# Kernel tuning notes

Measured on AMD Instinct MI355X. Metric: run time of the kernel, lower is better.

## Reference

```python
import jax, jax.numpy as jnp
import numpy as np

N = 100000          # nodes
E = 1600000         # edges (avg degree 16)
F_IN = 128          # num_node_features
H = 128             # hidden_channels
C = 8               # num_classes
EPS = 1e-5          # batchnorm eps
SLOPE = 0.01        # leaky_relu negative slope


def setup_inputs() -> dict:
    key = jax.random.key(0)
    ks = jax.random.split(key, 12)
    s = 0.05
    inp = {
        "node_feat": jax.random.normal(ks[0], (N, F_IN), jnp.float32),
        "src": jax.random.randint(ks[1], (E,), 0, N, dtype=jnp.int32),
        "dst": jax.random.randint(ks[2], (E,), 0, N, dtype=jnp.int32),
        # conv1 / conv2 (GraphConv weights + bias)
        "W1": jax.random.normal(ks[3], (F_IN, H), jnp.float32) * s,
        "b1": jnp.zeros((H,), jnp.float32),
        "W2": jax.random.normal(ks[4], (H, H), jnp.float32) * s,
        "b2": jnp.zeros((H,), jnp.float32),
        # batchnorm affine params
        "gamma1": jnp.ones((H,), jnp.float32),
        "beta1": jnp.zeros((H,), jnp.float32),
        "gamma2": jnp.ones((H,), jnp.float32),
        "beta2": jnp.zeros((H,), jnp.float32),
        # convnode1 / convnode2
        "Wn1": jax.random.normal(ks[5], (H, H), jnp.float32) * s,
        "bn1": jnp.zeros((H,), jnp.float32),
        "Wn2": jax.random.normal(ks[6], (H, H), jnp.float32) * s,
        "bn2": jnp.zeros((H,), jnp.float32),
        # node classifier
        "Wc": jax.random.normal(ks[7], (H, C), jnp.float32) * s,
        "bc": jnp.zeros((C,), jnp.float32),
    }
    return inp


def _deg_inv_sqrt(idx):
    # clamp(deg, min=1) ** -0.5, as in DGL GraphConv norm='both'
    deg = jax.ops.segment_sum(jnp.ones((E,), jnp.float32), idx, num_segments=N)
    return jnp.clip(deg, 1.0, None) ** -0.5


def _gconv(x, src, dst, W, b, out_norm, in_norm):
    # DGL GraphConv, norm='both': gather src-normalized feats, scatter-add to dst,
    # normalize by in-degree, then dense transform.
    msg = (x * out_norm[:, None])[src]                    # [E, d] gather
    agg = jax.ops.segment_sum(msg, dst, num_segments=N)   # [N, d] scatter-add
    return (agg * in_norm[:, None]) @ W + b


def _bn(x, gamma, beta):
    # training-mode BatchNorm1d: batch mean / biased var
    mean = jnp.mean(x, axis=0)
    var = jnp.var(x, axis=0)
    return (x - mean) * jax.lax.rsqrt(var + EPS) * gamma + beta


def _lrelu(x):
    return jnp.where(x >= 0, x, SLOPE * x)


def reference(node_feat, src, dst, W1, b1, W2, b2, gamma1, beta1, gamma2, beta2,
              Wn1, bn1, Wn2, bn2, Wc, bc):
    out_norm = _deg_inv_sqrt(src)   # src out-degree norm
    in_norm = _deg_inv_sqrt(dst)    # dst in-degree norm

    h = _gconv(node_feat, src, dst, W1, b1, out_norm, in_norm)
    h = _lrelu(_bn(h, gamma1, beta1))
    h = _gconv(h, src, dst, W2, b2, out_norm, in_norm)
    h = _lrelu(_bn(h, gamma2, beta2))

    hn = _lrelu(_gconv(h, src, dst, Wn1, bn1, out_norm, in_norm))
    hn = _lrelu(_gconv(hn, src, dst, Wn2, bn2, out_norm, in_norm))

    return hn @ Wc + bc   # [N, C]
```

## Files before the change

kernel.cpp:

```cpp
#include <hip/hip_runtime.h>
#include <math.h>

#define HN 128
#define NC 8
#define EPSV 1e-5f
#define SLOPEV 0.01f

typedef __attribute__((ext_vector_type(4))) float f32x4;
typedef __attribute__((ext_vector_type(8))) short bf16x8;

__device__ __forceinline__ uint bf16rne(float f) {
    uint u = __float_as_uint(f);
    return (u + 0x7fffu + ((u >> 16) & 1u)) >> 16;
}

__global__ __launch_bounds__(256) void rank_kernel(
        const int* __restrict__ src, const int* __restrict__ dst,
        int* __restrict__ degO, int* __restrict__ cntI,
        int* __restrict__ rnk, int E) {
    int base = blockIdx.x * 1024 + threadIdx.x;
    int s[4], d[4], r[4];
    #pragma unroll
    for (int k = 0; k < 4; k++) {
        int e = base + k * 256;
        if (e < E) { s[k] = src[e]; d[k] = dst[e]; }
    }
    #pragma unroll
    for (int k = 0; k < 4; k++) {
        int e = base + k * 256;
        if (e < E) atomicAdd(&degO[s[k]], 1);
    }
    #pragma unroll
    for (int k = 0; k < 4; k++) {
        int e = base + k * 256;
        if (e < E) r[k] = atomicAdd(&cntI[d[k]], 1);
    }
    #pragma unroll
    for (int k = 0; k < 4; k++) {
        int e = base + k * 256;
        if (e < E) rnk[e] = r[k];
    }
}

__global__ __launch_bounds__(256) void scan_partial(const int* __restrict__ degI,
                                                    int* __restrict__ blockSums, int n) {
    __shared__ int sS[256];
    int tid = threadIdx.x;
    int base = blockIdx.x * 1024 + tid * 4;
    int s = 0;
    #pragma unroll
    for (int j = 0; j < 4; j++) {
        int idx = base + j;
        s += (idx < n) ? degI[idx] : 0;
    }
    sS[tid] = s;
    __syncthreads();
    for (int off = 128; off; off >>= 1) {
        if (tid < off) sS[tid] += sS[tid + off];
        __syncthreads();
    }
    if (tid == 0) blockSums[blockIdx.x] = sS[0];
}

__global__ __launch_bounds__(1024) void scan_blocksums(int* __restrict__ blockSums, int nb) {
    __shared__ int sS[1024];
    int tid = threadIdx.x;
    int v = (tid < nb) ? blockSums[tid] : 0;
    sS[tid] = v;
    __syncthreads();
    for (int off = 1; off < 1024; off <<= 1) {
        int t = (tid >= off) ? sS[tid - off] : 0;
        __syncthreads();
        sS[tid] += t;
        __syncthreads();
    }
    if (tid < nb) blockSums[tid] = sS[tid] - v;
}

__global__ __launch_bounds__(256) void scan_final(const int* __restrict__ degI,
                                                  const int* __restrict__ degO,
                                                  const int* __restrict__ blockSums,
                                                  int* __restrict__ row_ptr,
                                                  float* __restrict__ onorm,
                                                  float* __restrict__ inorm, int n, int E) {
    __shared__ int sS[256];
    int tid = threadIdx.x;
    int base = blockIdx.x * 1024 + tid * 4;
    int v[4];
    int tot = 0;
    #pragma unroll
    for (int j = 0; j < 4; j++) {
        int idx = base + j;
        int vv = (idx < n) ? degI[idx] : 0;
        v[j] = tot;
        tot += vv;
    }
    sS[tid] = tot;
    __syncthreads();
    for (int off = 1; off < 256; off <<= 1) {
        int t = (tid >= off) ? sS[tid - off] : 0;
        __syncthreads();
        sS[tid] += t;
        __syncthreads();
    }
    int tb = blockSums[blockIdx.x] + sS[tid] - tot;
    #pragma unroll
    for (int j = 0; j < 4; j++) {
        int idx = base + j;
        if (idx < n) {
            row_ptr[idx] = tb + v[j];
            float a = (float)degO[idx]; if (a < 1.f) a = 1.f;
            float b = (float)degI[idx]; if (b < 1.f) b = 1.f;
            onorm[idx] = rsqrtf(a);
            inorm[idx] = rsqrtf(b);
        }
    }
    if (blockIdx.x == 0 && tid == 0) row_ptr[n] = E;
}

__global__ __launch_bounds__(256) void scatter_kernel(
        const int* __restrict__ src, const int* __restrict__ dst,
        const int* __restrict__ rnk, const int* __restrict__ row_ptr,
        int* __restrict__ srcs, int E) {
    int base = blockIdx.x * 1024 + threadIdx.x;
    int s[4], d[4], r[4], rp[4];
    #pragma unroll
    for (int k = 0; k < 4; k++) {
        int e = base + k * 256;
        if (e < E) { d[k] = dst[e]; r[k] = rnk[e]; s[k] = src[e]; }
    }
    #pragma unroll
    for (int k = 0; k < 4; k++) {
        int e = base + k * 256;
        if (e < E) rp[k] = row_ptr[d[k]];
    }
    #pragma unroll
    for (int k = 0; k < 4; k++) {
        int e = base + k * 256;
        if (e < E) srcs[rp[k] + r[k]] = s[k];
    }
}

__global__ __launch_bounds__(256) void wprep_kernel(
        const float* __restrict__ W1, const float* __restrict__ W2,
        const float* __restrict__ W3, const float* __restrict__ W4,
        ushort* __restrict__ WTh, ushort* __restrict__ WTl) {
    int i = blockIdx.x * blockDim.x + threadIdx.x;
    int l = i >> 14, r = i & 16383;
    int k = r >> 7, nn = r & 127;
    const float* W = (l == 0) ? W1 : (l == 1) ? W2 : (l == 2) ? W3 : W4;
    float w = W[k * HN + nn];
    uint hi = bf16rne(w);
    float fhi = __uint_as_float(hi << 16);
    uint lo = bf16rne(w - fhi);
    WTh[(size_t)l * 16384 + nn * HN + k] = (ushort)hi;
    WTl[(size_t)l * 16384 + nn * HN + k] = (ushort)lo;
}

__global__ __launch_bounds__(256) void pack_kernel(
        const float* __restrict__ in, const float* __restrict__ onorm,
        ushort* __restrict__ out, int total4) {
    int i = blockIdx.x * blockDim.x + threadIdx.x;
    if (i >= total4) return;
    float w = onorm[i >> 5];
    float4 v = ((const float4*)in)[i];
    ushort4 o = make_ushort4((ushort)bf16rne(v.x * w), (ushort)bf16rne(v.y * w),
                             (ushort)bf16rne(v.z * w), (ushort)bf16rne(v.w * w));
    *(ushort4*)(out + (size_t)i * 4) = o;
}

__global__ __launch_bounds__(256) void bnpack_kernel(
        const float* __restrict__ in, ushort* __restrict__ out,
        const float* __restrict__ scale, const float* __restrict__ shift,
        const float* __restrict__ onorm, int total4) {
    int i = blockIdx.x * blockDim.x + threadIdx.x;
    if (i >= total4) return;
    int cp = (i & 31) << 2;
    float w = onorm[i >> 5];
    float4 v = ((const float4*)in)[i];
    float4 s = *(const float4*)(scale + cp);
    float4 t = *(const float4*)(shift + cp);
    float h0 = fmaf(v.x, s.x, t.x); h0 = (h0 >= 0.f) ? h0 : SLOPEV * h0;
    float h1 = fmaf(v.y, s.y, t.y); h1 = (h1 >= 0.f) ? h1 : SLOPEV * h1;
    float h2 = fmaf(v.z, s.z, t.z); h2 = (h2 >= 0.f) ? h2 : SLOPEV * h2;
    float h3 = fmaf(v.w, s.w, t.w); h3 = (h3 >= 0.f) ? h3 : SLOPEV * h3;
    ushort4 o = make_ushort4((ushort)bf16rne(h0 * w), (ushort)bf16rne(h1 * w),
                             (ushort)bf16rne(h2 * w), (ushort)bf16rne(h3 * w));
    *(ushort4*)(out + (size_t)i * 4) = o;
}

__global__ __launch_bounds__(256) void agg_kernel(
        const uint* __restrict__ xb, uint* __restrict__ out,
        const int* __restrict__ srcs, const int* __restrict__ row_ptr,
        const float* __restrict__ inorm, int n) {
    int node = blockIdx.x * 4 + (threadIdx.x >> 6);
    if (node >= n) return;
    int lane = threadIdx.x & 63;
    int rp0 = row_ptr[node], rp1 = row_ptr[node + 1];
    float accx = 0.f, accy = 0.f;
    int j = rp0;
    for (; j + 3 < rp1; j += 4) {
        int s0 = srcs[j], s1 = srcs[j + 1], s2 = srcs[j + 2], s3 = srcs[j + 3];
        uint u0 = xb[(size_t)s0 * 64 + lane];
        uint u1 = xb[(size_t)s1 * 64 + lane];
        uint u2 = xb[(size_t)s2 * 64 + lane];
        uint u3 = xb[(size_t)s3 * 64 + lane];
        accx += __uint_as_float(u0 << 16) + __uint_as_float(u1 << 16)
              + __uint_as_float(u2 << 16) + __uint_as_float(u3 << 16);
        accy += __uint_as_float(u0 & 0xffff0000u) + __uint_as_float(u1 & 0xffff0000u)
              + __uint_as_float(u2 & 0xffff0000u) + __uint_as_float(u3 & 0xffff0000u);
    }
    for (; j < rp1; j++) {
        uint u0 = xb[(size_t)srcs[j] * 64 + lane];
        accx += __uint_as_float(u0 << 16);
        accy += __uint_as_float(u0 & 0xffff0000u);
    }
    float wi = inorm[node];
    uint o = bf16rne(accx * wi) | (bf16rne(accy * wi) << 16);
    out[(size_t)node * 64 + lane] = o;
}

template<int DO_STATS, int DO_LRELU, int DO_PACK, int DO_CLS>
__global__ __launch_bounds__(512) void gemm_mfma(
        const ushort* __restrict__ A, const uint4* __restrict__ WTh4,
        const uint4* __restrict__ WTl4, const float* __restrict__ bias,
        void* __restrict__ outv, float* __restrict__ colsum, float* __restrict__ colsq,
        const float* __restrict__ onorm,
        const float* __restrict__ Wc, const float* __restrict__ bc, int n) {
    __shared__ uint4 sW[4096];
    int tid = threadIdx.x;
    #pragma unroll
    for (int it = 0; it < 4; it++) {
        int j = it * 512 + tid;
        int nrow = j >> 4, c = j & 15;
        int sidx = nrow * 16 + (c ^ (nrow & 15));
        sW[sidx] = WTh4[j];
        sW[2048 + sidx] = WTl4[j];
    }
    __syncthreads();

    int wave = tid >> 6, lane = tid & 63;
    int l15 = lane & 15, quad = lane >> 4;
    int rbase = blockIdx.x * 128 + wave * 16;
    int arow = rbase + l15; if (arow > n - 1) arow = n - 1;

    bf16x8 af[4];
    #pragma unroll
    for (int kc = 0; kc < 4; kc++)
        af[kc] = *(const bf16x8*)(A + (size_t)arow * HN + kc * 32 + quad * 8);

    f32x4 acc[8];
    #pragma unroll
    for (int t = 0; t < 8; t++) acc[t] = (f32x4){0.f, 0.f, 0.f, 0.f};

    #pragma unroll
    for (int t = 0; t < 8; t++) {
        int nn = t * 16 + l15;
        int base = nn * 16, sw = nn & 15;
        #pragma unroll
        for (int kc = 0; kc < 4; kc++) {
            int c = kc * 4 + quad;
            bf16x8 bh = *(const bf16x8*)&sW[base + (c ^ sw)];
            acc[t] = __builtin_amdgcn_mfma_f32_16x16x32_bf16(af[kc], bh, acc[t], 0, 0, 0);
        }
        #pragma unroll
        for (int kc = 0; kc < 4; kc++) {
            int c = kc * 4 + quad;
            bf16x8 bl = *(const bf16x8*)&sW[2048 + base + (c ^ sw)];
            acc[t] = __builtin_amdgcn_mfma_f32_16x16x32_bf16(af[kc], bl, acc[t], 0, 0, 0);
        }
    }

    if (DO_CLS) {
        float bvt[8];
        #pragma unroll
        for (int t = 0; t < 8; t++) bvt[t] = bias[t * 16 + l15];
        #pragma unroll
        for (int c = 0; c < NC; c++) {
            float cl[4] = {0.f, 0.f, 0.f, 0.f};
            #pragma unroll
            for (int t = 0; t < 8; t++) {
                float wcv = Wc[(t * 16 + l15) * NC + c];
                #pragma unroll
                for (int i = 0; i < 4; i++) {
                    float v = acc[t][i] + bvt[t];
                    v = (v >= 0.f) ? v : SLOPEV * v;
                    cl[i] = fmaf(v, wcv, cl[i]);
                }
            }
            #pragma unroll
            for (int i = 0; i < 4; i++) {
                cl[i] += __shfl_xor(cl[i], 1);
                cl[i] += __shfl_xor(cl[i], 2);
                cl[i] += __shfl_xor(cl[i], 4);
                cl[i] += __shfl_xor(cl[i], 8);
            }
            if (l15 == 0) {
                float bcv = bc[c];
                #pragma unroll
                for (int i = 0; i < 4; i++) {
                    int row = rbase + quad * 4 + i;
                    if (row < n) ((float*)outv)[(size_t)row * NC + c] = cl[i] + bcv;
                }
            }
        }
        return;
    }

    float sarr[8], qarr[8];
    #pragma unroll
    for (int t = 0; t < 8; t++) {
        int col = t * 16 + l15;
        float bv = bias[col];
        float s = 0.f, q = 0.f;
        #pragma unroll
        for (int i = 0; i < 4; i++) {
            int row = rbase + quad * 4 + i;
            float v = acc[t][i] + bv;
            if (DO_LRELU) v = (v >= 0.f) ? v : SLOPEV * v;
            if (row < n) {
                if (DO_PACK) {
                    ((ushort*)outv)[(size_t)row * HN + col] = (ushort)bf16rne(v * onorm[row]);
                } else {
                    ((float*)outv)[(size_t)row * HN + col] = v;
                }
                if (DO_STATS) { s += v; q += v * v; }
            }
        }
        if (DO_STATS) {
            s += __shfl_xor(s, 16); q += __shfl_xor(q, 16);
            s += __shfl_xor(s, 32); q += __shfl_xor(q, 32);
        }
        sarr[t] = s; qarr[t] = q;
    }

    if (DO_STATS) {
        __syncthreads();
        float* sSum = (float*)sW;
        float* sSq  = (float*)sW + 1024;
        if (quad == 0) {
            #pragma unroll
            for (int t = 0; t < 8; t++) {
                sSum[wave * 128 + t * 16 + l15] = sarr[t];
                sSq [wave * 128 + t * 16 + l15] = qarr[t];
            }
        }
        __syncthreads();
        if (tid < 128) {
            float s = 0.f, q = 0.f;
            #pragma unroll
            for (int w = 0; w < 8; w++) { s += sSum[w * 128 + tid]; q += sSq[w * 128 + tid]; }
            atomicAdd(&colsum[tid], s);
            atomicAdd(&colsq[tid], q);
        }
    }
}

__global__ void bn_finalize(const float* __restrict__ colsum, const float* __restrict__ colsq,
                            const float* __restrict__ gamma, const float* __restrict__ beta,
                            float* __restrict__ scale, float* __restrict__ shift, int n) {
    int c = threadIdx.x;
    if (c < HN) {
        float inv = 1.f / (float)n;
        float mean = colsum[c] * inv;
        float var = colsq[c] * inv - mean * mean;
        if (var < 0.f) var = 0.f;
        float s = gamma[c] * rsqrtf(var + EPSV);
        scale[c] = s;
        shift[c] = beta[c] - mean * s;
    }
}

extern "C" void kernel_launch(void* const* d_in, const int* in_sizes, int n_in,
                              void* d_out, int out_size, void* d_ws, size_t ws_size,
                              hipStream_t stream) {
    const float* node_feat = (const float*)d_in[0];
    const int*   src    = (const int*)d_in[1];
    const int*   dst    = (const int*)d_in[2];
    const float* W1     = (const float*)d_in[3];
    const float* b1     = (const float*)d_in[4];
    const float* W2     = (const float*)d_in[5];
    const float* b2     = (const float*)d_in[6];
    const float* gamma1 = (const float*)d_in[7];
    const float* beta1  = (const float*)d_in[8];
    const float* gamma2 = (const float*)d_in[9];
    const float* beta2  = (const float*)d_in[10];
    const float* Wn1    = (const float*)d_in[11];
    const float* bn1    = (const float*)d_in[12];
    const float* Wn2    = (const float*)d_in[13];
    const float* bn2    = (const float*)d_in[14];
    const float* Wc     = (const float*)d_in[15];
    const float* bc     = (const float*)d_in[16];
    float* out = (float*)d_out;

    const int N = in_sizes[0] / HN;
    const int E = in_sizes[1];

    char* p = (char*)d_ws;
    float* bufA  = (float*)p; p += (size_t)N * HN * 4;
    float* bufB  = (float*)p; p += (size_t)N * HN * 4;
    float* onorm = (float*)p; p += (size_t)N * 4;
    float* inorm = (float*)p; p += (size_t)N * 4;
    float* scale = (float*)p; p += HN * 4;
    float* shift = (float*)p; p += HN * 4;
    char* zbase = p;
    float* cs1 = (float*)p; p += HN * 4;
    float* cq1 = (float*)p; p += HN * 4;
    float* cs2 = (float*)p; p += HN * 4;
    float* cq2 = (float*)p; p += HN * 4;
    int* degO = (int*)p; p += (size_t)N * 4;
    int* cntI = (int*)p; p += (size_t)N * 4;
    size_t zbytes = (size_t)(p - zbase);
    int* row_ptr = (int*)p; p += (size_t)(N + 4) * 4;
    int* blockSums = (int*)p; p += 1024 * 4;
    int* rnk     = (int*)p; p += (size_t)E * 4;
    int* srcs    = (int*)p; p += (size_t)E * 4;
    ushort* WTh  = (ushort*)p; p += 4 * 16384 * 2;
    ushort* WTl  = (ushort*)p; p += 4 * 16384 * 2;
    if ((size_t)(p - (char*)d_ws) > ws_size) return;

    hipMemsetAsync(zbase, 0, zbytes, stream);

    int gE4 = (E + 1023) / 1024;
    int nb = (N + 1023) / 1024;
    rank_kernel<<<gE4, 256, 0, stream>>>(src, dst, degO, cntI, rnk, E);
    scan_partial<<<nb, 256, 0, stream>>>(cntI, blockSums, N);
    scan_blocksums<<<1, 1024, 0, stream>>>(blockSums, nb);
    scan_final<<<nb, 256, 0, stream>>>(cntI, degO, blockSums, row_ptr, onorm, inorm, N, E);
    scatter_kernel<<<gE4, 256, 0, stream>>>(src, dst, rnk, row_ptr, srcs, E);
    wprep_kernel<<<256, 256, 0, stream>>>(W1, W2, Wn1, Wn2, WTh, WTl);

    int gAgg = (N + 3) / 4;
    int gGemm = (N + 127) / 128;
    int gApply = (N * 32 + 255) / 256;

    ushort* HbA = (ushort*)bufA;
    ushort* Abf = (ushort*)bufA + (size_t)N * HN;
    ushort* HbB = (ushort*)bufB;

    pack_kernel<<<gApply, 256, 0, stream>>>(node_feat, onorm, HbA, N * 32);
    agg_kernel<<<gAgg, 256, 0, stream>>>((const uint*)HbA, (uint*)Abf, srcs, row_ptr, inorm, N);
    gemm_mfma<1, 0, 0, 0><<<gGemm, 512, 0, stream>>>(Abf, (const uint4*)WTh, (const uint4*)WTl,
                                                     b1, bufB, cs1, cq1, nullptr, nullptr, nullptr, N);
    bn_finalize<<<1, 128, 0, stream>>>(cs1, cq1, gamma1, beta1, scale, shift, N);
    bnpack_kernel<<<gApply, 256, 0, stream>>>(bufB, HbA, scale, shift, onorm, N * 32);

    agg_kernel<<<gAgg, 256, 0, stream>>>((const uint*)HbA, (uint*)Abf, srcs, row_ptr, inorm, N);
    gemm_mfma<1, 0, 0, 0><<<gGemm, 512, 0, stream>>>(Abf, (const uint4*)(WTh + 16384),
                                                     (const uint4*)(WTl + 16384),
                                                     b2, bufB, cs2, cq2, nullptr, nullptr, nullptr, N);
    bn_finalize<<<1, 128, 0, stream>>>(cs2, cq2, gamma2, beta2, scale, shift, N);
    bnpack_kernel<<<gApply, 256, 0, stream>>>(bufB, HbA, scale, shift, onorm, N * 32);

    agg_kernel<<<gAgg, 256, 0, stream>>>((const uint*)HbA, (uint*)Abf, srcs, row_ptr, inorm, N);
    gemm_mfma<0, 1, 1, 0><<<gGemm, 512, 0, stream>>>(Abf, (const uint4*)(WTh + 2 * 16384),
                                                     (const uint4*)(WTl + 2 * 16384),
                                                     bn1, HbB, nullptr, nullptr, onorm, nullptr, nullptr, N);

    agg_kernel<<<gAgg, 256, 0, stream>>>((const uint*)HbB, (uint*)Abf, srcs, row_ptr, inorm, N);
    gemm_mfma<0, 0, 0, 1><<<gGemm, 512, 0, stream>>>(Abf, (const uint4*)(WTh + 3 * 16384),
                                                     (const uint4*)(WTl + 3 * 16384),
                                                     bn2, out, nullptr, nullptr, nullptr, Wc, bc, N);
}
```

Before: 799.8 us.

## Split packed features into two column halves and use per-XCC degree counters

Packed bf16 feature buffers are stored as two planar 64-column halves, so each aggregation pass gathers 128-byte rows from one half at a time. Work is split across twice as many blocks, each wave handling two edges per step with 32 lanes each and combining via a cross-lane shuffle. The intent is a smaller gather working set per pass, for better L2 reuse and more memory parallelism. Out-degree counting is also privatized per XCC using workgroup-scope atomics, with the eight copies summed in scan_final, to cut cross-die atomic traffic. The risks are more index arithmetic, half-wasted lanes on low-degree nodes, and atomic-scope correctness relying on the XCC ID register.

```diff
diff --git a/kernel.cpp b/kernel.cpp
--- a/kernel.cpp
+++ b/kernel.cpp
@@ -14,10 +14,17 @@
     return (u + 0x7fffu + ((u >> 16) & 1u)) >> 16;
 }
 
+__device__ __forceinline__ int xcc_id() {
+    int x;
+    asm volatile("s_getreg_b32 %0, hwreg(HW_REG_XCC_ID)" : "=s"(x));
+    return x & 7;
+}
+
 __global__ __launch_bounds__(256) void rank_kernel(
         const int* __restrict__ src, const int* __restrict__ dst,
-        int* __restrict__ degO, int* __restrict__ cntI,
-        int* __restrict__ rnk, int E) {
+        int* __restrict__ degO8, int* __restrict__ cntI,
+        int* __restrict__ rnk, int E, int n) {
+    int* myDeg = degO8 + (size_t)xcc_id() * n;
     int base = blockIdx.x * 1024 + threadIdx.x;
     int s[4], d[4], r[4];
     #pragma unroll
@@ -28,7 +35,9 @@
     #pragma unroll
     for (int k = 0; k < 4; k++) {
         int e = base + k * 256;
-        if (e < E) atomicAdd(&degO[s[k]], 1);
+        if (e < E)
+            __hip_atomic_fetch_add(&myDeg[s[k]], 1, __ATOMIC_RELAXED,
+                                   __HIP_MEMORY_SCOPE_WORKGROUP);
     }
     #pragma unroll
     for (int k = 0; k < 4; k++) {
@@ -78,7 +87,7 @@
 }
 
 __global__ __launch_bounds__(256) void scan_final(const int* __restrict__ degI,
-                                                  const int* __restrict__ degO,
+                                                  const int* __restrict__ degO8,
                                                   const int* __restrict__ blockSums,
                                                   int* __restrict__ row_ptr,
                                                   float* __restrict__ onorm,
@@ -109,7 +118,10 @@
         int idx = base + j;
         if (idx < n) {
             row_ptr[idx] = tb + v[j];
-            float a = (float)degO[idx]; if (a < 1.f) a = 1.f;
+            int dsum = 0;
+            #pragma unroll
+            for (int s8 = 0; s8 < 8; s8++) dsum += degO8[(size_t)s8 * n + idx];
+            float a = (float)dsum; if (a < 1.f) a = 1.f;
             float b = (float)degI[idx]; if (b < 1.f) b = 1.f;
             onorm[idx] = rsqrtf(a);
             inorm[idx] = rsqrtf(b);
@@ -159,24 +171,27 @@
 
 __global__ __launch_bounds__(256) void pack_kernel(
         const float* __restrict__ in, const float* __restrict__ onorm,
-        ushort* __restrict__ out, int total4) {
+        ushort* __restrict__ out, int nrows) {
     int i = blockIdx.x * blockDim.x + threadIdx.x;
-    if (i >= total4) return;
-    float w = onorm[i >> 5];
+    if (i >= nrows * 32) return;
+    int row = i >> 5, q4 = i & 31;
+    float w = onorm[row];
     float4 v = ((const float4*)in)[i];
     ushort4 o = make_ushort4((ushort)bf16rne(v.x * w), (ushort)bf16rne(v.y * w),
                              (ushort)bf16rne(v.z * w), (ushort)bf16rne(v.w * w));
-    *(ushort4*)(out + (size_t)i * 4) = o;
+    int h = q4 >> 4, lc = (q4 * 2) & 31;
+    *(ushort4*)(out + (((size_t)h * nrows + row) * 32 + lc) * 2) = o;
 }
 
 __global__ __launch_bounds__(256) void bnpack_kernel(
         const float* __restrict__ in, ushort* __restrict__ out,
         const float* __restrict__ scale, const float* __restrict__ shift,
-        const float* __restrict__ onorm, int total4) {
+        const float* __restrict__ onorm, int nrows) {
     int i = blockIdx.x * blockDim.x + threadIdx.x;
-    if (i >= total4) return;
-    int cp = (i & 31) << 2;
-    float w = onorm[i >> 5];
+    if (i >= nrows * 32) return;
+    int row = i >> 5, q4 = i & 31;
+    int cp = q4 << 2;
+    float w = onorm[row];
     float4 v = ((const float4*)in)[i];
     float4 s = *(const float4*)(scale + cp);
     float4 t = *(const float4*)(shift + cp);
@@ -186,38 +201,46 @@
     float h3 = fmaf(v.w, s.w, t.w); h3 = (h3 >= 0.f) ? h3 : SLOPEV * h3;
     ushort4 o = make_ushort4((ushort)bf16rne(h0 * w), (ushort)bf16rne(h1 * w),
                              (ushort)bf16rne(h2 * w), (ushort)bf16rne(h3 * w));
-    *(ushort4*)(out + (size_t)i * 4) = o;
+    int h = q4 >> 4, lc = (q4 * 2) & 31;
+    *(ushort4*)(out + (((size_t)h * nrows + row) * 32 + lc) * 2) = o;
 }
 
 __global__ __launch_bounds__(256) void agg_kernel(
-        const uint* __restrict__ xb, uint* __restrict__ out,
+        const uint* __restrict__ xb, uint* __restrict__ outb,
         const int* __restrict__ srcs, const int* __restrict__ row_ptr,
-        const float* __restrict__ inorm, int n) {
-    int node = blockIdx.x * 4 + (threadIdx.x >> 6);
+        const float* __restrict__ inorm, int n, int nodeBlocks) {
+    int h = blockIdx.x / nodeBlocks;
+    int nb = blockIdx.x - h * nodeBlocks;
+    int node = nb * 4 + (threadIdx.x >> 6);
     if (node >= n) return;
     int lane = threadIdx.x & 63;
+    int g = lane >> 5, li = lane & 31;
+    const uint* Q = xb + (size_t)h * n * 32;
     int rp0 = row_ptr[node], rp1 = row_ptr[node + 1];
     float accx = 0.f, accy = 0.f;
-    int j = rp0;
-    for (; j + 3 < rp1; j += 4) {
-        int s0 = srcs[j], s1 = srcs[j + 1], s2 = srcs[j + 2], s3 = srcs[j + 3];
-        uint u0 = xb[(size_t)s0 * 64 + lane];
-        uint u1 = xb[(size_t)s1 * 64 + lane];
-        uint u2 = xb[(size_t)s2 * 64 + lane];
-        uint u3 = xb[(size_t)s3 * 64 + lane];
+    int j = rp0 + g;
+    for (; j + 6 < rp1; j += 8) {
+        int s0 = srcs[j], s1 = srcs[j + 2], s2 = srcs[j + 4], s3 = srcs[j + 6];
+        uint u0 = Q[(size_t)s0 * 32 + li];
+        uint u1 = Q[(size_t)s1 * 32 + li];
+        uint u2 = Q[(size_t)s2 * 32 + li];
+        uint u3 = Q[(size_t)s3 * 32 + li];
         accx += __uint_as_float(u0 << 16) + __uint_as_float(u1 << 16)
               + __uint_as_float(u2 << 16) + __uint_as_float(u3 << 16);
         accy += __uint_as_float(u0 & 0xffff0000u) + __uint_as_float(u1 & 0xffff0000u)
               + __uint_as_float(u2 & 0xffff0000u) + __uint_as_float(u3 & 0xffff0000u);
     }
-    for (; j < rp1; j++) {
-        uint u0 = xb[(size_t)srcs[j] * 64 + lane];
+    for (; j < rp1; j += 2) {
+        uint u0 = Q[(size_t)srcs[j] * 32 + li];
         accx += __uint_as_float(u0 << 16);
         accy += __uint_as_float(u0 & 0xffff0000u);
     }
-    float wi = inorm[node];
-    uint o = bf16rne(accx * wi) | (bf16rne(accy * wi) << 16);
-    out[(size_t)node * 64 + lane] = o;
+    accx += __shfl_xor(accx, 32); accy += __shfl_xor(accy, 32);
+    if (g == 0) {
+        float wi = inorm[node];
+        uint o = bf16rne(accx * wi) | (bf16rne(accy * wi) << 16);
+        outb[((size_t)h * n + node) * 32 + li] = o;
+    }
 }
 
 template<int DO_STATS, int DO_LRELU, int DO_PACK, int DO_CLS>
@@ -246,8 +269,10 @@
 
     bf16x8 af[4];
     #pragma unroll
-    for (int kc = 0; kc < 4; kc++)
-        af[kc] = *(const bf16x8*)(A + (size_t)arow * HN + kc * 32 + quad * 8);
+    for (int kc = 0; kc < 4; kc++) {
+        int c0 = kc * 32 + quad * 8;
+        af[kc] = *(const bf16x8*)(A + ((size_t)(c0 >> 6) * n + arow) * 64 + (c0 & 63));
+    }
 
     f32x4 acc[8];
     #pragma unroll
@@ -320,7 +345,8 @@
             if (DO_LRELU) v = (v >= 0.f) ? v : SLOPEV * v;
             if (row < n) {
                 if (DO_PACK) {
-                    ((ushort*)outv)[(size_t)row * HN + col] = (ushort)bf16rne(v * onorm[row]);
+                    ((ushort*)outv)[((size_t)(col >> 6) * n + row) * 64 + (col & 63)] =
+                        (ushort)bf16rne(v * onorm[row]);
                 } else {
                     ((float*)outv)[(size_t)row * HN + col] = v;
                 }
@@ -408,8 +434,8 @@
     float* cq1 = (float*)p; p += HN * 4;
     float* cs2 = (float*)p; p += HN * 4;
     float* cq2 = (float*)p; p += HN * 4;
-    int* degO = (int*)p; p += (size_t)N * 4;
-    int* cntI = (int*)p; p += (size_t)N * 4;
+    int* cntI  = (int*)p; p += (size_t)N * 4;
+    int* degO8 = (int*)p; p += (size_t)8 * N * 4;
     size_t zbytes = (size_t)(p - zbase);
     int* row_ptr = (int*)p; p += (size_t)(N + 4) * 4;
     int* blockSums = (int*)p; p += 1024 * 4;
@@ -423,14 +449,15 @@
 
     int gE4 = (E + 1023) / 1024;
     int nb = (N + 1023) / 1024;
-    rank_kernel<<<gE4, 256, 0, stream>>>(src, dst, degO, cntI, rnk, E);
+    rank_kernel<<<gE4, 256, 0, stream>>>(src, dst, degO8, cntI, rnk, E, N);
     scan_partial<<<nb, 256, 0, stream>>>(cntI, blockSums, N);
     scan_blocksums<<<1, 1024, 0, stream>>>(blockSums, nb);
-    scan_final<<<nb, 256, 0, stream>>>(cntI, degO, blockSums, row_ptr, onorm, inorm, N, E);
+    scan_final<<<nb, 256, 0, stream>>>(cntI, degO8, blockSums, row_ptr, onorm, inorm, N, E);
     scatter_kernel<<<gE4, 256, 0, stream>>>(src, dst, rnk, row_ptr, srcs, E);
     wprep_kernel<<<256, 256, 0, stream>>>(W1, W2, Wn1, Wn2, WTh, WTl);
 
-    int gAgg = (N + 3) / 4;
+    int nodeBlocks = (N + 3) / 4;
+    int gAgg = nodeBlocks * 2;
     int gGemm = (N + 127) / 128;
     int gApply = (N * 32 + 255) / 256;
 
@@ -438,26 +465,26 @@
     ushort* Abf = (ushort*)bufA + (size_t)N * HN;
     ushort* HbB = (ushort*)bufB;
 
-    pack_kernel<<<gApply, 256, 0, stream>>>(node_feat, onorm, HbA, N * 32);
-    agg_kernel<<<gAgg, 256, 0, stream>>>((const uint*)HbA, (uint*)Abf, srcs, row_ptr, inorm, N);
+    pack_kernel<<<gApply, 256, 0, stream>>>(node_feat, onorm, HbA, N);
+    agg_kernel<<<gAgg, 256, 0, stream>>>((const uint*)HbA, (uint*)Abf, srcs, row_ptr, inorm, N, nodeBlocks);
     gemm_mfma<1, 0, 0, 0><<<gGemm, 512, 0, stream>>>(Abf, (const uint4*)WTh, (const uint4*)WTl,
                                                      b1, bufB, cs1, cq1, nullptr, nullptr, nullptr, N);
     bn_finalize<<<1, 128, 0, stream>>>(cs1, cq1, gamma1, beta1, scale, shift, N);
-    bnpack_kernel<<<gApply, 256, 0, stream>>>(bufB, HbA, scale, shift, onorm, N * 32);
-
-    agg_kernel<<<gAgg, 256, 0, stream>>>((const uint*)HbA, (uint*)Abf, srcs, row_ptr, inorm, N);
+    bnpack_kernel<<<gApply, 256, 0, stream>>>(bufB, HbA, scale, shift, onorm, N);
+
+    agg_kernel<<<gAgg, 256, 0, stream>>>((const uint*)HbA, (uint*)Abf, srcs, row_ptr, inorm, N, nodeBlocks);
     gemm_mfma<1, 0, 0, 0><<<gGemm, 512, 0, stream>>>(Abf, (const uint4*)(WTh + 16384),
                                                      (const uint4*)(WTl + 16384),
                                                      b2, bufB, cs2, cq2, nullptr, nullptr, nullptr, N);
     bn_finalize<<<1, 128, 0, stream>>>(cs2, cq2, gamma2, beta2, scale, shift, N);
-    bnpack_kernel<<<gApply, 256, 0, stream>>>(bufB, HbA, scale, shift, onorm, N * 32);
-
-    agg_kernel<<<gAgg, 256, 0, stream>>>((const uint*)HbA, (uint*)Abf, srcs, row_ptr, inorm, N);
+    bnpack_kernel<<<gApply, 256, 0, stream>>>(bufB, HbA, scale, shift, onorm, N);
+
+    agg_kernel<<<gAgg, 256, 0, stream>>>((const uint*)HbA, (uint*)Abf, srcs, row_ptr, inorm, N, nodeBlocks);
     gemm_mfma<0, 1, 1, 0><<<gGemm, 512, 0, stream>>>(Abf, (const uint4*)(WTh + 2 * 16384),
                                                      (const uint4*)(WTl + 2 * 16384),
                                                      bn1, HbB, nullptr, nullptr, onorm, nullptr, nullptr, N);
 
-    agg_kernel<<<gAgg, 256, 0, stream>>>((const uint*)HbB, (uint*)Abf, srcs, row_ptr, inorm, N);
+    agg_kernel<<<gAgg, 256, 0, stream>>>((const uint*)HbB, (uint*)Abf, srcs, row_ptr, inorm, N, nodeBlocks);
     gemm_mfma<0, 0, 0, 1><<<gGemm, 512, 0, stream>>>(Abf, (const uint4*)(WTh + 3 * 16384),
                                                      (const uint4*)(WTl + 3 * 16384),
                                                      bn2, out, nullptr, nullptr, nullptr, Wc, bc, N);
```

Measured after the change: 915.7 us. 1.15x slower.

## Privatize degree and rank atomics per XCD to avoid cross-die atomic traffic

Applied to the files above, without the earlier changes.

Replaces the global degree and in-count atomics with eight per-XCD copies, indexed by the hardware XCC id and updated with workgroup-scope relaxed atomics so they can resolve in each die's L2. Rank values carry the XCD id in their upper bits. Per-XCD prefix offsets are then built in scan_final and used in the scatter to place edges in CSR order. This adds eight times the counter memory and memset, plus extra reads in the scan kernels. It also relies on workgroup-scope atomics being coherent across all CUs of one XCD, which is a correctness risk.

```diff
diff --git a/kernel.cpp b/kernel.cpp
--- a/kernel.cpp
+++ b/kernel.cpp
@@ -14,10 +14,19 @@
     return (u + 0x7fffu + ((u >> 16) & 1u)) >> 16;
 }
 
+__device__ __forceinline__ int xcc_id() {
+    int x;
+    asm volatile("s_getreg_b32 %0, hwreg(HW_REG_XCC_ID)" : "=s"(x));
+    return x & 7;
+}
+
 __global__ __launch_bounds__(256) void rank_kernel(
         const int* __restrict__ src, const int* __restrict__ dst,
-        int* __restrict__ degO, int* __restrict__ cntI,
-        int* __restrict__ rnk, int E) {
+        int* __restrict__ degO8, int* __restrict__ cntI8,
+        int* __restrict__ rnk, int E, int n) {
+    int x = xcc_id();
+    int* myDeg = degO8 + (size_t)x * n;
+    int* myCnt = cntI8 + (size_t)x * n;
     int base = blockIdx.x * 1024 + threadIdx.x;
     int s[4], d[4], r[4];
     #pragma unroll
@@ -28,21 +37,25 @@
     #pragma unroll
     for (int k = 0; k < 4; k++) {
         int e = base + k * 256;
-        if (e < E) atomicAdd(&degO[s[k]], 1);
-    }
-    #pragma unroll
-    for (int k = 0; k < 4; k++) {
-        int e = base + k * 256;
-        if (e < E) r[k] = atomicAdd(&cntI[d[k]], 1);
-    }
-    #pragma unroll
-    for (int k = 0; k < 4; k++) {
-        int e = base + k * 256;
-        if (e < E) rnk[e] = r[k];
-    }
-}
-
-__global__ __launch_bounds__(256) void scan_partial(const int* __restrict__ degI,
+        if (e < E)
+            __hip_atomic_fetch_add(&myDeg[s[k]], 1, __ATOMIC_RELAXED,
+                                   __HIP_MEMORY_SCOPE_WORKGROUP);
+    }
+    #pragma unroll
+    for (int k = 0; k < 4; k++) {
+        int e = base + k * 256;
+        if (e < E)
+            r[k] = __hip_atomic_fetch_add(&myCnt[d[k]], 1, __ATOMIC_RELAXED,
+                                          __HIP_MEMORY_SCOPE_WORKGROUP);
+    }
+    #pragma unroll
+    for (int k = 0; k < 4; k++) {
+        int e = base + k * 256;
+        if (e < E) rnk[e] = (x << 28) | r[k];
+    }
+}
+
+__global__ __launch_bounds__(256) void scan_partial(const int* __restrict__ cntI8,
                                                     int* __restrict__ blockSums, int n) {
     __shared__ int sS[256];
     int tid = threadIdx.x;
@@ -51,7 +64,10 @@
     #pragma unroll
     for (int j = 0; j < 4; j++) {
         int idx = base + j;
-        s += (idx < n) ? degI[idx] : 0;
+        if (idx < n) {
+            #pragma unroll
+            for (int x = 0; x < 8; x++) s += cntI8[(size_t)x * n + idx];
+        }
     }
     sS[tid] = s;
     __syncthreads();
@@ -77,10 +93,11 @@
     if (tid < nb) blockSums[tid] = sS[tid] - v;
 }
 
-__global__ __launch_bounds__(256) void scan_final(const int* __restrict__ degI,
-                                                  const int* __restrict__ degO,
+__global__ __launch_bounds__(256) void scan_final(const int* __restrict__ cntI8,
+                                                  const int* __restrict__ degO8,
                                                   const int* __restrict__ blockSums,
                                                   int* __restrict__ row_ptr,
+                                                  int* __restrict__ xcdoff8,
                                                   float* __restrict__ onorm,
                                                   float* __restrict__ inorm, int n, int E) {
     __shared__ int sS[256];
@@ -91,9 +108,16 @@
     #pragma unroll
     for (int j = 0; j < 4; j++) {
         int idx = base + j;
-        int vv = (idx < n) ? degI[idx] : 0;
+        int deg = 0;
+        if (idx < n) {
+            #pragma unroll
+            for (int x = 0; x < 8; x++) {
+                xcdoff8[(size_t)x * n + idx] = deg;
+                deg += cntI8[(size_t)x * n + idx];
+            }
+        }
         v[j] = tot;
-        tot += vv;
+        tot += deg;
     }
     sS[tid] = tot;
     __syncthreads();
@@ -104,13 +128,21 @@
         __syncthreads();
     }
     int tb = blockSums[blockIdx.x] + sS[tid] - tot;
+    int run = 0;
     #pragma unroll
     for (int j = 0; j < 4; j++) {
         int idx = base + j;
         if (idx < n) {
-            row_ptr[idx] = tb + v[j];
-            float a = (float)degO[idx]; if (a < 1.f) a = 1.f;
-            float b = (float)degI[idx]; if (b < 1.f) b = 1.f;
+            row_ptr[idx] = tb + run;
+            int deg = 0, dO = 0;
+            #pragma unroll
+            for (int x = 0; x < 8; x++) {
+                deg += cntI8[(size_t)x * n + idx];
+                dO  += degO8[(size_t)x * n + idx];
+            }
+            run += deg;
+            float a = (float)dO; if (a < 1.f) a = 1.f;
+            float b = (float)deg; if (b < 1.f) b = 1.f;
             onorm[idx] = rsqrtf(a);
             inorm[idx] = rsqrtf(b);
         }
@@ -121,9 +153,9 @@
 __global__ __launch_bounds__(256) void scatter_kernel(
         const int* __restrict__ src, const int* __restrict__ dst,
         const int* __restrict__ rnk, const int* __restrict__ row_ptr,
-        int* __restrict__ srcs, int E) {
+        const int* __restrict__ xcdoff8, int* __restrict__ srcs, int E, int n) {
     int base = blockIdx.x * 1024 + threadIdx.x;
-    int s[4], d[4], r[4], rp[4];
+    int s[4], d[4], r[4], rp[4], xo[4];
     #pragma unroll
     for (int k = 0; k < 4; k++) {
         int e = base + k * 256;
@@ -132,12 +164,15 @@
     #pragma unroll
     for (int k = 0; k < 4; k++) {
         int e = base + k * 256;
-        if (e < E) rp[k] = row_ptr[d[k]];
-    }
-    #pragma unroll
-    for (int k = 0; k < 4; k++) {
-        int e = base + k * 256;
-        if (e < E) srcs[rp[k] + r[k]] = s[k];
+        if (e < E) {
+            rp[k] = row_ptr[d[k]];
+            xo[k] = xcdoff8[(size_t)(r[k] >> 28) * n + d[k]];
+        }
+    }
+    #pragma unroll
+    for (int k = 0; k < 4; k++) {
+        int e = base + k * 256;
+        if (e < E) srcs[rp[k] + xo[k] + (r[k] & 0x0FFFFFFF)] = s[k];
     }
 }
 
@@ -408,9 +443,10 @@
     float* cq1 = (float*)p; p += HN * 4;
     float* cs2 = (float*)p; p += HN * 4;
     float* cq2 = (float*)p; p += HN * 4;
-    int* degO = (int*)p; p += (size_t)N * 4;
-    int* cntI = (int*)p; p += (size_t)N * 4;
+    int* degO8 = (int*)p; p += (size_t)8 * N * 4;
+    int* cntI8 = (int*)p; p += (size_t)8 * N * 4;
     size_t zbytes = (size_t)(p - zbase);
+    int* xcdoff8 = (int*)p; p += (size_t)8 * N * 4;
     int* row_ptr = (int*)p; p += (size_t)(N + 4) * 4;
     int* blockSums = (int*)p; p += 1024 * 4;
     int* rnk     = (int*)p; p += (size_t)E * 4;
@@ -423,11 +459,12 @@
 
     int gE4 = (E + 1023) / 1024;
     int nb = (N + 1023) / 1024;
-    rank_kernel<<<gE4, 256, 0, stream>>>(src, dst, degO, cntI, rnk, E);
-    scan_partial<<<nb, 256, 0, stream>>>(cntI, blockSums, N);
+    rank_kernel<<<gE4, 256, 0, stream>>>(src, dst, degO8, cntI8, rnk, E, N);
+    scan_partial<<<nb, 256, 0, stream>>>(cntI8, blockSums, N);
     scan_blocksums<<<1, 1024, 0, stream>>>(blockSums, nb);
-    scan_final<<<nb, 256, 0, stream>>>(cntI, degO, blockSums, row_ptr, onorm, inorm, N, E);
-    scatter_kernel<<<gE4, 256, 0, stream>>>(src, dst, rnk, row_ptr, srcs, E);
+    scan_final<<<nb, 256, 0, stream>>>(cntI8, degO8, blockSums, row_ptr, xcdoff8,
+                                       onorm, inorm, N, E);
+    scatter_kernel<<<gE4, 256, 0, stream>>>(src, dst, rnk, row_ptr, xcdoff8, srcs, E, N);
     wprep_kernel<<<256, 256, 0, stream>>>(W1, W2, Wn1, Wn2, WTh, WTl);
 
     int gAgg = (N + 3) / 4;
```

Result: no change. 801.6 us (+0.2%).

## Privatize out-degree counts per XCC and split edge gather across half-waves

Applied to the files above, without the earlier changes.

Out-degree counting now uses eight per-XCC copies of the degree array, incremented with workgroup-scope relaxed atomics, and scan_final sums the eight copies. This aims to avoid cross-die atomic traffic. The aggregation kernel has each half-wave handle alternate edges with 8-byte loads per lane, then combines the halves with a cross-lane shuffle. This keeps more independent gathers in flight per wave. The cost is a larger memset and extra reads in scan_final, and workgroup-scope atomics are only correct if all blocks sharing a copy go to the same XCC's L2.

```diff
diff --git a/kernel.cpp b/kernel.cpp
--- a/kernel.cpp
+++ b/kernel.cpp
@@ -14,10 +14,20 @@
     return (u + 0x7fffu + ((u >> 16) & 1u)) >> 16;
 }
 
+__device__ __forceinline__ float blo(uint u) { return __uint_as_float(u << 16); }
+__device__ __forceinline__ float bhi(uint u) { return __uint_as_float(u & 0xffff0000u); }
+
+__device__ __forceinline__ int xcc_id() {
+    int x;
+    asm volatile("s_getreg_b32 %0, hwreg(HW_REG_XCC_ID)" : "=s"(x));
+    return x & 7;
+}
+
 __global__ __launch_bounds__(256) void rank_kernel(
         const int* __restrict__ src, const int* __restrict__ dst,
-        int* __restrict__ degO, int* __restrict__ cntI,
-        int* __restrict__ rnk, int E) {
+        int* __restrict__ degO8, int* __restrict__ cntI,
+        int* __restrict__ rnk, int E, int n) {
+    int* myDeg = degO8 + (size_t)xcc_id() * n;
     int base = blockIdx.x * 1024 + threadIdx.x;
     int s[4], d[4], r[4];
     #pragma unroll
@@ -28,7 +38,9 @@
     #pragma unroll
     for (int k = 0; k < 4; k++) {
         int e = base + k * 256;
-        if (e < E) atomicAdd(&degO[s[k]], 1);
+        if (e < E)
+            __hip_atomic_fetch_add(&myDeg[s[k]], 1, __ATOMIC_RELAXED,
+                                   __HIP_MEMORY_SCOPE_WORKGROUP);
     }
     #pragma unroll
     for (int k = 0; k < 4; k++) {
@@ -78,7 +90,7 @@
 }
 
 __global__ __launch_bounds__(256) void scan_final(const int* __restrict__ degI,
-                                                  const int* __restrict__ degO,
+                                                  const int* __restrict__ degO8,
                                                   const int* __restrict__ blockSums,
                                                   int* __restrict__ row_ptr,
                                                   float* __restrict__ onorm,
@@ -109,7 +121,10 @@
         int idx = base + j;
         if (idx < n) {
             row_ptr[idx] = tb + v[j];
-            float a = (float)degO[idx]; if (a < 1.f) a = 1.f;
+            int dsum = 0;
+            #pragma unroll
+            for (int s8 = 0; s8 < 8; s8++) dsum += degO8[(size_t)s8 * n + idx];
+            float a = (float)dsum; if (a < 1.f) a = 1.f;
             float b = (float)degI[idx]; if (b < 1.f) b = 1.f;
             onorm[idx] = rsqrtf(a);
             inorm[idx] = rsqrtf(b);
@@ -190,34 +205,41 @@
 }
 
 __global__ __launch_bounds__(256) void agg_kernel(
-        const uint* __restrict__ xb, uint* __restrict__ out,
+        const uint2* __restrict__ xb2, uint2* __restrict__ out2,
         const int* __restrict__ srcs, const int* __restrict__ row_ptr,
         const float* __restrict__ inorm, int n) {
     int node = blockIdx.x * 4 + (threadIdx.x >> 6);
     if (node >= n) return;
     int lane = threadIdx.x & 63;
+    int g = lane >> 5, li = lane & 31;
     int rp0 = row_ptr[node], rp1 = row_ptr[node + 1];
-    float accx = 0.f, accy = 0.f;
-    int j = rp0;
-    for (; j + 3 < rp1; j += 4) {
-        int s0 = srcs[j], s1 = srcs[j + 1], s2 = srcs[j + 2], s3 = srcs[j + 3];
-        uint u0 = xb[(size_t)s0 * 64 + lane];
-        uint u1 = xb[(size_t)s1 * 64 + lane];
-        uint u2 = xb[(size_t)s2 * 64 + lane];
-        uint u3 = xb[(size_t)s3 * 64 + lane];
-        accx += __uint_as_float(u0 << 16) + __uint_as_float(u1 << 16)
-              + __uint_as_float(u2 << 16) + __uint_as_float(u3 << 16);
-        accy += __uint_as_float(u0 & 0xffff0000u) + __uint_as_float(u1 & 0xffff0000u)
-              + __uint_as_float(u2 & 0xffff0000u) + __uint_as_float(u3 & 0xffff0000u);
-    }
-    for (; j < rp1; j++) {
-        uint u0 = xb[(size_t)srcs[j] * 64 + lane];
-        accx += __uint_as_float(u0 << 16);
-        accy += __uint_as_float(u0 & 0xffff0000u);
-    }
-    float wi = inorm[node];
-    uint o = bf16rne(accx * wi) | (bf16rne(accy * wi) << 16);
-    out[(size_t)node * 64 + lane] = o;
+    float a0 = 0.f, a1 = 0.f, a2 = 0.f, a3 = 0.f;
+    int j = rp0 + g;
+    for (; j + 6 < rp1; j += 8) {
+        int s0 = srcs[j], s1 = srcs[j + 2], s2 = srcs[j + 4], s3 = srcs[j + 6];
+        uint2 u0 = xb2[(size_t)s0 * 32 + li];
+        uint2 u1 = xb2[(size_t)s1 * 32 + li];
+        uint2 u2 = xb2[(size_t)s2 * 32 + li];
+        uint2 u3 = xb2[(size_t)s3 * 32 + li];
+        a0 += blo(u0.x) + blo(u1.x) + blo(u2.x) + blo(u3.x);
+        a1 += bhi(u0.x) + bhi(u1.x) + bhi(u2.x) + bhi(u3.x);
+        a2 += blo(u0.y) + blo(u1.y) + blo(u2.y) + blo(u3.y);
+        a3 += bhi(u0.y) + bhi(u1.y) + bhi(u2.y) + bhi(u3.y);
+    }
+    for (; j < rp1; j += 2) {
+        uint2 u = xb2[(size_t)srcs[j] * 32 + li];
+        a0 += blo(u.x); a1 += bhi(u.x);
+        a2 += blo(u.y); a3 += bhi(u.y);
+    }
+    a0 += __shfl_xor(a0, 32); a1 += __shfl_xor(a1, 32);
+    a2 += __shfl_xor(a2, 32); a3 += __shfl_xor(a3, 32);
+    if (g == 0) {
+        float wi = inorm[node];
+        uint2 o;
+        o.x = bf16rne(a0 * wi) | (bf16rne(a1 * wi) << 16);
+        o.y = bf16rne(a2 * wi) | (bf16rne(a3 * wi) << 16);
+        out2[(size_t)node * 32 + li] = o;
+    }
 }
 
 template<int DO_STATS, int DO_LRELU, int DO_PACK, int DO_CLS>
@@ -408,8 +430,8 @@
     float* cq1 = (float*)p; p += HN * 4;
     float* cs2 = (float*)p; p += HN * 4;
     float* cq2 = (float*)p; p += HN * 4;
-    int* degO = (int*)p; p += (size_t)N * 4;
-    int* cntI = (int*)p; p += (size_t)N * 4;
+    int* degO8 = (int*)p; p += (size_t)8 * N * 4;
+    int* cntI  = (int*)p; p += (size_t)N * 4;
     size_t zbytes = (size_t)(p - zbase);
     int* row_ptr = (int*)p; p += (size_t)(N + 4) * 4;
     int* blockSums = (int*)p; p += 1024 * 4;
@@ -423,10 +445,10 @@
 
     int gE4 = (E + 1023) / 1024;
     int nb = (N + 1023) / 1024;
-    rank_kernel<<<gE4, 256, 0, stream>>>(src, dst, degO, cntI, rnk, E);
+    rank_kernel<<<gE4, 256, 0, stream>>>(src, dst, degO8, cntI, rnk, E, N);
     scan_partial<<<nb, 256, 0, stream>>>(cntI, blockSums, N);
     scan_blocksums<<<1, 1024, 0, stream>>>(blockSums, nb);
-    scan_final<<<nb, 256, 0, stream>>>(cntI, degO, blockSums, row_ptr, onorm, inorm, N, E);
+    scan_final<<<nb, 256, 0, stream>>>(cntI, degO8, blockSums, row_ptr, onorm, inorm, N, E);
     scatter_kernel<<<gE4, 256, 0, stream>>>(src, dst, rnk, row_ptr, srcs, E);
     wprep_kernel<<<256, 256, 0, stream>>>(W1, W2, Wn1, Wn2, WTh, WTl);
 
@@ -439,25 +461,25 @@
     ushort* HbB = (ushort*)bufB;
 
     pack_kernel<<<gApply, 256, 0, stream>>>(node_feat, onorm, HbA, N * 32);
-    agg_kernel<<<gAgg, 256, 0, stream>>>((const uint*)HbA, (uint*)Abf, srcs, row_ptr, inorm, N);
+    agg_kernel<<<gAgg, 256, 0, stream>>>((const uint2*)HbA, (uint2*)Abf, srcs, row_ptr, inorm, N);
     gemm_mfma<1, 0, 0, 0><<<gGemm, 512, 0, stream>>>(Abf, (const uint4*)WTh, (const uint4*)WTl,
                                                      b1, bufB, cs1, cq1, nullptr, nullptr, nullptr, N);
     bn_finalize<<<1, 128, 0, stream>>>(cs1, cq1, gamma1, beta1, scale, shift, N);
     bnpack_kernel<<<gApply, 256, 0, stream>>>(bufB, HbA, scale, shift, onorm, N * 32);
 
-    agg_kernel<<<gAgg, 256, 0, stream>>>((const uint*)HbA, (uint*)Abf, srcs, row_ptr, inorm, N);
+    agg_kernel<<<gAgg, 256, 0, stream>>>((const uint2*)HbA, (uint2*)Abf, srcs, row_ptr, inorm, N);
     gemm_mfma<1, 0, 0, 0><<<gGemm, 512, 0, stream>>>(Abf, (const uint4*)(WTh + 16384),
                                                      (const uint4*)(WTl + 16384),
                                                      b2, bufB, cs2, cq2, nullptr, nullptr, nullptr, N);
     bn_finalize<<<1, 128, 0, stream>>>(cs2, cq2, gamma2, beta2, scale, shift, N);
     bnpack_kernel<<<gApply, 256, 0, stream>>>(bufB, HbA, scale, shift, onorm, N * 32);
 
-    agg_kernel<<<gAgg, 256, 0, stream>>>((const uint*)HbA, (uint*)Abf, srcs, row_ptr, inorm, N);
+    agg_kernel<<<gAgg, 256, 0, stream>>>((const uint2*)HbA, (uint2*)Abf, srcs, row_ptr, inorm, N);
     gemm_mfma<0, 1, 1, 0><<<gGemm, 512, 0, stream>>>(Abf, (const uint4*)(WTh + 2 * 16384),
                                                      (const uint4*)(WTl + 2 * 16384),
                                                      bn1, HbB, nullptr, nullptr, onorm, nullptr, nullptr, N);
 
-    agg_kernel<<<gAgg, 256, 0, stream>>>((const uint*)HbB, (uint*)Abf, srcs, row_ptr, inorm, N);
+    agg_kernel<<<gAgg, 256, 0, stream>>>((const uint2*)HbB, (uint2*)Abf, srcs, row_ptr, inorm, N);
     gemm_mfma<0, 0, 0, 1><<<gGemm, 512, 0, stream>>>(Abf, (const uint4*)(WTh + 3 * 16384),
                                                      (const uint4*)(WTl + 3 * 16384),
                                                      bn2, out, nullptr, nullptr, nullptr, Wc, bc, N);
```

After: 743.5 us. 7.0% less time.
